# Kernel optimization log

Hardware: AMD Instinct MI355X
Metric: run time of the kernel (lower is better)

The kernel has to match this reference:

```python
import jax, jax.numpy as jnp
import numpy as np
import itertools

N = 600000
CIN = 64
COUT = 64
KS = 3
STRIDE = 2
DIL = 1
GRID = 256        # coordinate range before striding
M = 512           # per-axis key radix (fits int32 keys for batch<=2)
SHIFT = (KS - 1) // 2 * DIL   # keeps shifted coords non-negative under neighbor offsets
SENT = 2 ** 30    # sentinel key for padded unique slots
BN_EPS = 1e-5

OFFSETS = list(itertools.product(range(-(KS // 2), KS // 2 + 1), repeat=3))  # 27 offsets, row-major


def setup_inputs() -> dict:
    key = jax.random.key(0)
    k1, k2, k3, k4, k5, k6, k7, k8 = jax.random.split(key, 8)
    xyz = jax.random.randint(k1, (N, 3), 0, GRID, dtype=jnp.int32)
    b = jax.random.randint(k2, (N, 1), 0, 2, dtype=jnp.int32)  # batch of 2 scenes
    coords = jnp.concatenate([xyz, b], axis=1)                 # [N,4] = (x,y,z,batch)
    feats = jax.random.normal(k3, (N, CIN), dtype=jnp.float32)
    weight = jax.random.normal(k4, (27, CIN, COUT), dtype=jnp.float32) / np.sqrt(27 * CIN)
    bn_scale = jax.random.uniform(k5, (COUT,), jnp.float32, 0.5, 1.5)
    bn_bias = jax.random.normal(k6, (COUT,), jnp.float32) * 0.1
    bn_mean = jax.random.normal(k7, (COUT,), jnp.float32) * 0.1
    bn_var = jax.random.uniform(k8, (COUT,), jnp.float32, 0.5, 1.5)
    return {"coords": coords, "feats": feats, "weight": weight,
            "bn_scale": bn_scale, "bn_bias": bn_bias, "bn_mean": bn_mean, "bn_var": bn_var}


def _encode(xyz, b):
    # pack (batch, x, y, z) into a single sortable int32 key
    return ((b * M + xyz[:, 0] + SHIFT) * M + (xyz[:, 1] + SHIFT)) * M + (xyz[:, 2] + SHIFT)


def _forward(coords, feats, weight, bn_scale, bn_bias, bn_mean, bn_var):
    # --- stride path: voxel downsample via unique + scatter-add (index_add) ---
    xyz = coords[:, :3] // STRIDE
    b = coords[:, 3]
    keys = _encode(xyz, b)                                   # [N]
    ukeys, inv = jnp.unique(keys, size=N, fill_value=SENT, return_inverse=True)  # sorted, padded
    fds = jax.ops.segment_sum(feats, inv, num_segments=N)    # pooled feats [N, CIN]
    valid = ukeys < SENT                                      # real (non-padded) voxels

    # --- sparse 3x3x3 conv at stride 1 (output coords == input coords) ---
    # gather(neighbor) -> matmul(W_k) -> accumulate, per kernel offset
    out = jnp.zeros((N, COUT), dtype=feats.dtype)
    for k, (dx, dy, dz) in enumerate(OFFSETS):
        delta = ((dx * M) + dy) * M + dz
        q = ukeys + delta * DIL
        pos = jnp.clip(jnp.searchsorted(ukeys, q), 0, N - 1)
        match = (ukeys[pos] == q) & valid
        gathered = jnp.where(match[:, None], fds[pos], 0.0)   # [N, CIN]
        out = out + gathered @ weight[k]

    # --- BatchNorm (eval-mode running stats) + ReLU ---
    inv_std = jax.lax.rsqrt(bn_var + BN_EPS)
    out = (out - bn_mean) * (bn_scale * inv_std) + bn_bias
    out = jax.nn.relu(out)
    return jnp.where(valid[:, None], out, 0.0)                # zero padded rows


def reference(coords, feats, weight, bn_scale, bn_bias, bn_mean, bn_var):
    return _forward(coords, feats, weight, bn_scale, bn_bias, bn_mean, bn_var)
```

## Files before the change

kernel.cpp:

```cpp
#include <hip/hip_runtime.h>
#include <hip/hip_bf16.h>

#define NPTS 600000
#define NKEYS (1 << 22)
#define CHUNK 4096
#define NPART (NKEYS / CHUNK)

typedef unsigned int u32;
typedef unsigned short u16;
typedef __attribute__((ext_vector_type(8))) short short8;
typedef __attribute__((ext_vector_type(4))) float f32x4;

__device__ __forceinline__ u16 f2bf(float x) {
  union { float f; u32 u; } c; c.f = x;
  u32 r = c.u + 0x7fffu + ((c.u >> 16) & 1u);
  return (u16)(r >> 16);
}

__global__ void k0a_bn(const float* __restrict__ s, const float* __restrict__ b,
                       const float* __restrict__ m, const float* __restrict__ v,
                       float* __restrict__ ab) {
  int c = threadIdx.x;
  float a = s[c] * rsqrtf(v[c] + 1e-5f);
  ab[c] = a;
  ab[64 + c] = b[c] - m[c] * a;
}

__global__ void k0b_wt(const float* __restrict__ W, u16* __restrict__ Wt) {
  int e = blockIdx.x * 256 + threadIdx.x;
  if (e >= 27 * 4096) return;
  int k = e >> 12, rem = e & 4095, cin = rem >> 6, cout = rem & 63;
  Wt[(k << 12) + (cout << 6) + cin] = f2bf(W[e]);
}

__global__ void k1_keys(const int* __restrict__ coords, int* __restrict__ keys,
                        u32* __restrict__ lut) {
  int i = blockIdx.x * 256 + threadIdx.x;
  if (i >= NPTS) return;
  int4 c4 = *(const int4*)(coords + i * 4);
  int k = (c4.w << 21) | ((c4.x >> 1) << 14) | ((c4.y >> 1) << 7) | (c4.z >> 1);
  keys[i] = k;
  atomicAdd(&lut[k], 1u);
}

__global__ void k2a_part(const u32* __restrict__ lut, u32* __restrict__ partials) {
  __shared__ u32 sd[256];
  int blk = blockIdx.x, t = threadIdx.x;
  const u32* p = lut + blk * CHUNK;
  u32 s = 0;
  for (int j = t; j < CHUNK; j += 256) s += (p[j] != 0u);
  sd[t] = s; __syncthreads();
  for (int o = 128; o > 0; o >>= 1) { if (t < o) sd[t] += sd[t + o]; __syncthreads(); }
  if (t == 0) partials[blk] = sd[0];
}

__global__ void k2b_top(u32* __restrict__ partials) {
  __shared__ u32 sh[NPART];
  int t = threadIdx.x;
  u32 x = partials[t];
  sh[t] = x; __syncthreads();
  for (int off = 1; off < NPART; off <<= 1) {
    u32 add = (t >= off) ? sh[t - off] : 0u;
    __syncthreads();
    sh[t] += add;
    __syncthreads();
  }
  partials[t] = sh[t] - x;
  if (t == NPART - 1) partials[NPART] = sh[t];
}

__global__ void k2c_fill(u32* __restrict__ lut, const u32* __restrict__ partials,
                         int* __restrict__ r2k, float* __restrict__ fds32) {
  __shared__ u32 tsum[256];
  int blk = blockIdx.x, t = threadIdx.x;
  int base = blk * CHUNK + t * 16;
  u32 loc[16]; u32 s = 0;
#pragma unroll
  for (int j = 0; j < 16; j++) { loc[j] = lut[base + j]; s += (loc[j] != 0u); }
  tsum[t] = s; __syncthreads();
  for (int off = 1; off < 256; off <<= 1) {
    u32 add = (t >= off) ? tsum[t - off] : 0u;
    __syncthreads();
    tsum[t] += add;
    __syncthreads();
  }
  u32 rank = partials[blk] + tsum[t] - s;
#pragma unroll
  for (int j = 0; j < 16; j++) {
    if (loc[j]) {
      u32 flag = (loc[j] > 1u) ? 0x80000000u : 0u;
      lut[base + j] = (rank + 1u) | flag;
      r2k[rank] = base + j;
      if (flag) {
        float4 z = {0.f, 0.f, 0.f, 0.f};
        float* d = fds32 + ((size_t)rank << 6);
#pragma unroll
        for (int c = 0; c < 16; c++) *(float4*)(d + c * 4) = z;
      }
      rank++;
    } else lut[base + j] = 0u;
  }
}

__global__ void k3_seg(const float* __restrict__ feats, const int* __restrict__ keys,
                       const u32* __restrict__ lut, float* __restrict__ fds32,
                       u16* __restrict__ fdsb) {
  int idx = blockIdx.x * 256 + threadIdx.x;
  if (idx >= NPTS * 16) return;
  int i = idx >> 4, q = (idx & 15) << 2;
  u32 lv = lut[keys[i]];
  u32 r = (lv & 0x7fffffffu) - 1u;
  float4 v = *(const float4*)(feats + (size_t)i * 64 + q);
  if (lv >> 31) {
    float* dst = fds32 + ((size_t)r << 6) + q;
    atomicAdd(dst + 0, v.x); atomicAdd(dst + 1, v.y);
    atomicAdd(dst + 2, v.z); atomicAdd(dst + 3, v.w);
  } else {
    ushort4 o;
    o.x = f2bf(v.x); o.y = f2bf(v.y); o.z = f2bf(v.z); o.w = f2bf(v.w);
    *(ushort4*)(fdsb + ((size_t)r << 6) + q) = o;
  }
}

__global__ void k3b_fix(const int* __restrict__ r2k, const u32* __restrict__ lut,
                        const u32* __restrict__ pU,
                        const float* __restrict__ fds32, u16* __restrict__ fdsb) {
  int idx = blockIdx.x * 256 + threadIdx.x;
  int r = idx >> 2;
  if (r >= (int)(*pU)) return;
  u32 lv = lut[r2k[r]];
  if (!(lv >> 31)) return;
  int q = (idx & 3) << 4;
  const float* src = fds32 + ((size_t)r << 6) + q;
  u16* dst = fdsb + ((size_t)r << 6) + q;
#pragma unroll
  for (int j = 0; j < 4; j++) {
    float4 v = *(const float4*)(src + j * 4);
    ushort4 o;
    o.x = f2bf(v.x); o.y = f2bf(v.y); o.z = f2bf(v.z); o.w = f2bf(v.w);
    *(ushort4*)(dst + j * 4) = o;
  }
}

__global__ __launch_bounds__(320) void k4_conv(
    const u32* __restrict__ lut, const int* __restrict__ r2k,
    const u16* __restrict__ fdsb, const u16* __restrict__ Wt,
    const u32* __restrict__ pU, const float* __restrict__ ab,
    float* __restrict__ out) {
  __shared__ __align__(16) char ldsA[2][8192];
  const u32 U = *pU;
  int tid = threadIdx.x;
  int w = tid >> 6, l = tid & 63;
  int bid = blockIdx.x;
  int cpx = (int)gridDim.x >> 3;
  int swz = (bid & 7) * cpx + (bid >> 3);
  int rbase = swz * 64;

  int key = -1, x = 0, y = 0, z = 0;
  if (w == 0) {
    int r = rbase + l;
    key = ((u32)r < U) ? r2k[r] : -1;
    z = key & 127; y = (key >> 7) & 127; x = (key >> 14) & 127;
  }
  u32 lvr[4];
  short8 rg[2][8];
  const short8 z8 = {0, 0, 0, 0, 0, 0, 0, 0};

#define PROBE(T) { \
    const int dx_ = (T) / 9 - 1, dy_ = ((T) / 3) % 3 - 1, dz_ = (T) % 3 - 1; \
    int nx_ = x + dx_, ny_ = y + dy_, nz_ = z + dz_; \
    bool ok_ = (key >= 0) & ((u32)nx_ < 128u) & ((u32)ny_ < 128u) & ((u32)nz_ < 128u); \
    int a_ = ok_ ? (key + dx_ * 16384 + dy_ * 128 + dz_) : NKEYS; \
    lvr[(T) & 3] = lut[a_]; }

#define LOADRG(T) { \
    u32 lv_ = lvr[(T) & 3]; \
    _Pragma("unroll") for (int j = 0; j < 8; j++) rg[(T) & 1][j] = z8; \
    if (lv_) { \
      const u16* fr_ = fdsb + ((size_t)((lv_ & 0x7fffffffu) - 1u) << 6); \
      _Pragma("unroll") for (int j = 0; j < 8; j++) \
        rg[(T) & 1][j] = *(const short8*)(fr_ + j * 8); } }

#define DSW(T) { \
    char* dst_ = &ldsA[(T) & 1][l * 128]; \
    int r7_ = l & 7; \
    _Pragma("unroll") for (int j = 0; j < 8; j++) \
      *(short8*)(dst_ + (((j + r7_) & 7) << 4)) = rg[(T) & 1][j]; }

  int ct = w - 1;
  int col = l & 15, kg = l >> 4;
  f32x4 acc[4] = {};

  if (w == 0) {
    PROBE(0) PROBE(1) PROBE(2) PROBE(3)
    LOADRG(0)
    DSW(0)
    LOADRG(1)
  }
  asm volatile("" ::: "memory");
  asm volatile("s_waitcnt lgkmcnt(0)" ::: "memory");
  __builtin_amdgcn_s_barrier();
  asm volatile("" ::: "memory");

#pragma unroll
  for (int k = 0; k < 27; k++) {
    if (w == 0) {
      if (k + 1 < 27) DSW(k + 1)
      if (k + 2 < 27) LOADRG(k + 2)
      if (k + 4 < 27) PROBE(k + 4)
    } else {
      const u16* wk = Wt + (k << 12) + (((ct << 4) + col) << 6) + (kg << 3);
      short8 b0 = *(const short8*)(wk);
      short8 b1 = *(const short8*)(wk + 32);
      const char* slab = &ldsA[k & 1][0];
#pragma unroll
      for (int rt = 0; rt < 4; rt++) {
        int row = (rt << 4) + col;
        const char* rp = slab + row * 128;
        int r7 = row & 7;
        short8 a0 = *(const short8*)(rp + (((kg + r7) & 7) << 4));
        short8 a1 = *(const short8*)(rp + (((kg + 4 + r7) & 7) << 4));
        acc[rt] = __builtin_amdgcn_mfma_f32_16x16x32_bf16(a0, b0, acc[rt], 0, 0, 0);
        acc[rt] = __builtin_amdgcn_mfma_f32_16x16x32_bf16(a1, b1, acc[rt], 0, 0, 0);
      }
    }
    asm volatile("" ::: "memory");
    asm volatile("s_waitcnt lgkmcnt(0)" ::: "memory");
    __builtin_amdgcn_s_barrier();
    asm volatile("" ::: "memory");
  }
#undef PROBE
#undef LOADRG
#undef DSW

  if (w > 0) {
    int c = (ct << 4) | col;
    float al = ab[c], be = ab[64 + c];
#pragma unroll
    for (int rt = 0; rt < 4; rt++) {
#pragma unroll
      for (int i = 0; i < 4; i++) {
        int r = rbase + (rt << 4) + (kg << 2) + i;
        if (r >= NPTS) continue;
        bool valid = ((u32)r < U);
        float vv = 0.f;
        if (valid) {
          vv = fmaf(acc[rt][i], al, be);
          vv = vv > 0.f ? vv : 0.f;
        }
        out[((size_t)r << 6) + c] = vv;
      }
    }
  }
}

extern "C" void kernel_launch(void* const* d_in, const int* in_sizes, int n_in,
                              void* d_out, int out_size, void* d_ws, size_t ws_size,
                              hipStream_t stream) {
  const int*   coords = (const int*)d_in[0];
  const float* feats  = (const float*)d_in[1];
  const float* W      = (const float*)d_in[2];
  const float* bns    = (const float*)d_in[3];
  const float* bnb    = (const float*)d_in[4];
  const float* bnm    = (const float*)d_in[5];
  const float* bnv    = (const float*)d_in[6];
  float* out = (float*)d_out;

  char* ws = (char*)d_ws;
  size_t off = 0;
  auto alloc = [&](size_t bytes) -> void* {
    void* p = ws + off;
    off += (bytes + 255) & ~(size_t)255;
    return p;
  };
  u32* lut      = (u32*)alloc((size_t)(NKEYS + 1) * 4);
  u32* partials = (u32*)alloc((NPART + 8) * 4);
  int* keys     = (int*)alloc((size_t)NPTS * 4);
  int* r2k      = (int*)alloc((size_t)NPTS * 4);
  u16* fdsb     = (u16*)alloc((size_t)(NPTS + 1) * 64 * 2);
  u16* Wt       = (u16*)alloc((size_t)27 * 4096 * 2);
  float* ab     = (float*)alloc(128 * 4);
  (void)ws_size; (void)out_size; (void)n_in; (void)in_sizes;

  float* fds32 = out;

  hipMemsetAsync(lut, 0, (size_t)(NKEYS + 1) * 4, stream);

  k0a_bn<<<1, 64, 0, stream>>>(bns, bnb, bnm, bnv, ab);
  k0b_wt<<<(27 * 4096 + 255) / 256, 256, 0, stream>>>(W, Wt);
  k1_keys<<<(NPTS + 255) / 256, 256, 0, stream>>>(coords, keys, lut);
  k2a_part<<<NPART, 256, 0, stream>>>(lut, partials);
  k2b_top<<<1, NPART, 0, stream>>>(partials);
  k2c_fill<<<NPART, 256, 0, stream>>>(lut, partials, r2k, fds32);
  k3_seg<<<(NPTS * 16 + 255) / 256, 256, 0, stream>>>(feats, keys, lut, fds32, fdsb);
  k3b_fix<<<(NPTS * 4 + 255) / 256, 256, 0, stream>>>(r2k, lut, partials + NPART, fds32, fdsb);
  k4_conv<<<(NPTS + 63) / 64, 320, 0, stream>>>(lut, r2k, fdsb, Wt,
                                                partials + NPART, ab, out);
}
```

Measured before the change: 590.8 us.

## Use direct global-to-LDS loads with a 5-stage ring for conv gathers

The producer wave now issues buffer global_load_lds instructions that write gathered neighbor feature rows straight into LDS, replacing the register round trip and separate LDS store. The double buffer becomes a five-slot ring so loads run three offsets ahead, tracked by explicit vmcnt waits. Rows with no neighbor point at a zeroed pad row, which removes the branch. The LDS layout changes from a swizzled row-major form to a column-chunk-major form that matches the direct-load pattern. LDS use grows to 40KB per block, which may lower occupancy, and the hand-counted waits are fragile.

```diff
diff --git a/kernel.cpp b/kernel.cpp
--- a/kernel.cpp
+++ b/kernel.cpp
@@ -147,7 +147,7 @@
     const u16* __restrict__ fdsb, const u16* __restrict__ Wt,
     const u32* __restrict__ pU, const float* __restrict__ ab,
     float* __restrict__ out) {
-  __shared__ __align__(16) char ldsA[2][8192];
+  __shared__ __align__(16) char ldsA[5][8192];
   const u32 U = *pU;
   int tid = threadIdx.x;
   int w = tid >> 6, l = tid & 63;
@@ -163,8 +163,6 @@
     z = key & 127; y = (key >> 7) & 127; x = (key >> 14) & 127;
   }
   u32 lvr[4];
-  short8 rg[2][8];
-  const short8 z8 = {0, 0, 0, 0, 0, 0, 0, 0};
 
 #define PROBE(T) { \
     const int dx_ = (T) / 9 - 1, dy_ = ((T) / 3) % 3 - 1, dz_ = (T) % 3 - 1; \
@@ -173,65 +171,74 @@
     int a_ = ok_ ? (key + dx_ * 16384 + dy_ * 128 + dz_) : NKEYS; \
     lvr[(T) & 3] = lut[a_]; }
 
-#define LOADRG(T) { \
+#define GLD(T) { \
     u32 lv_ = lvr[(T) & 3]; \
-    _Pragma("unroll") for (int j = 0; j < 8; j++) rg[(T) & 1][j] = z8; \
-    if (lv_) { \
-      const u16* fr_ = fdsb + ((size_t)((lv_ & 0x7fffffffu) - 1u) << 6); \
-      _Pragma("unroll") for (int j = 0; j < 8; j++) \
-        rg[(T) & 1][j] = *(const short8*)(fr_ + j * 8); } }
-
-#define DSW(T) { \
-    char* dst_ = &ldsA[(T) & 1][l * 128]; \
-    int r7_ = l & 7; \
-    _Pragma("unroll") for (int j = 0; j < 8; j++) \
-      *(short8*)(dst_ + (((j + r7_) & 7) << 4)) = rg[(T) & 1][j]; }
+    u32 row_ = lv_ ? ((lv_ & 0x7fffffffu) - 1u) : (u32)NPTS; \
+    const char* fr_ = (const char*)(fdsb + ((size_t)row_ << 6)); \
+    char* sl_ = &ldsA[(T) % 5][0]; \
+    __builtin_amdgcn_global_load_lds((const __attribute__((address_space(1))) void*)(fr_ +   0), (__attribute__((address_space(3))) void*)(sl_ +    0), 16, 0, 0); \
+    __builtin_amdgcn_global_load_lds((const __attribute__((address_space(1))) void*)(fr_ +  16), (__attribute__((address_space(3))) void*)(sl_ + 1024), 16, 0, 0); \
+    __builtin_amdgcn_global_load_lds((const __attribute__((address_space(1))) void*)(fr_ +  32), (__attribute__((address_space(3))) void*)(sl_ + 2048), 16, 0, 0); \
+    __builtin_amdgcn_global_load_lds((const __attribute__((address_space(1))) void*)(fr_ +  48), (__attribute__((address_space(3))) void*)(sl_ + 3072), 16, 0, 0); \
+    __builtin_amdgcn_global_load_lds((const __attribute__((address_space(1))) void*)(fr_ +  64), (__attribute__((address_space(3))) void*)(sl_ + 4096), 16, 0, 0); \
+    __builtin_amdgcn_global_load_lds((const __attribute__((address_space(1))) void*)(fr_ +  80), (__attribute__((address_space(3))) void*)(sl_ + 5120), 16, 0, 0); \
+    __builtin_amdgcn_global_load_lds((const __attribute__((address_space(1))) void*)(fr_ +  96), (__attribute__((address_space(3))) void*)(sl_ + 6144), 16, 0, 0); \
+    __builtin_amdgcn_global_load_lds((const __attribute__((address_space(1))) void*)(fr_ + 112), (__attribute__((address_space(3))) void*)(sl_ + 7168), 16, 0, 0); }
 
   int ct = w - 1;
   int col = l & 15, kg = l >> 4;
   f32x4 acc[4] = {};
 
+#define CONSUME(K) { \
+    const char* sl_ = &ldsA[(K) % 5][0]; \
+    const u16* wk_ = Wt + ((K) << 12) + (((ct << 4) + col) << 6) + (kg << 3); \
+    short8 b0_ = *(const short8*)(wk_); \
+    short8 b1_ = *(const short8*)(wk_ + 32); \
+    short8 a0_[4], a1_[4]; \
+    _Pragma("unroll") for (int rt = 0; rt < 4; rt++) { \
+      int row_ = (rt << 4) + col; \
+      a0_[rt] = *(const short8*)(sl_ + (kg << 10) + (row_ << 4)); \
+      a1_[rt] = *(const short8*)(sl_ + ((kg + 4) << 10) + (row_ << 4)); } \
+    _Pragma("unroll") for (int rt = 0; rt < 4; rt++) { \
+      acc[rt] = __builtin_amdgcn_mfma_f32_16x16x32_bf16(a0_[rt], b0_, acc[rt], 0, 0, 0); \
+      acc[rt] = __builtin_amdgcn_mfma_f32_16x16x32_bf16(a1_[rt], b1_, acc[rt], 0, 0, 0); } }
+
+#define NWAIT(K) ( (((K)-1) < 24 ? 8 : 0) + (((K)-1) < 21 ? 1 : 0) + \
+                   (((K)     < 24) ? 8 : 0) + (((K)     < 21) ? 1 : 0) )
+
+#define BODY(K) { \
+    if (w == 0) { \
+      if ((K) + 3 < 27) GLD((K) + 3) \
+      if ((K) + 6 < 27) PROBE((K) + 6) \
+      asm volatile("s_waitcnt vmcnt(%0)" :: "n"(NWAIT(K)) : "memory"); \
+    } else { \
+      CONSUME(K) \
+    } \
+    asm volatile("" ::: "memory"); \
+    __builtin_amdgcn_s_barrier(); \
+    asm volatile("" ::: "memory"); }
+
   if (w == 0) {
     PROBE(0) PROBE(1) PROBE(2) PROBE(3)
-    LOADRG(0)
-    DSW(0)
-    LOADRG(1)
+    asm volatile("s_waitcnt vmcnt(0)" ::: "memory");
+    GLD(0)
+    asm volatile("s_waitcnt vmcnt(0)" ::: "memory");
+    PROBE(4) GLD(1) PROBE(5) GLD(2)
   }
   asm volatile("" ::: "memory");
-  asm volatile("s_waitcnt lgkmcnt(0)" ::: "memory");
   __builtin_amdgcn_s_barrier();
   asm volatile("" ::: "memory");
 
-#pragma unroll
-  for (int k = 0; k < 27; k++) {
-    if (w == 0) {
-      if (k + 1 < 27) DSW(k + 1)
-      if (k + 2 < 27) LOADRG(k + 2)
-      if (k + 4 < 27) PROBE(k + 4)
-    } else {
-      const u16* wk = Wt + (k << 12) + (((ct << 4) + col) << 6) + (kg << 3);
-      short8 b0 = *(const short8*)(wk);
-      short8 b1 = *(const short8*)(wk + 32);
-      const char* slab = &ldsA[k & 1][0];
-#pragma unroll
-      for (int rt = 0; rt < 4; rt++) {
-        int row = (rt << 4) + col;
-        const char* rp = slab + row * 128;
-        int r7 = row & 7;
-        short8 a0 = *(const short8*)(rp + (((kg + r7) & 7) << 4));
-        short8 a1 = *(const short8*)(rp + (((kg + 4 + r7) & 7) << 4));
-        acc[rt] = __builtin_amdgcn_mfma_f32_16x16x32_bf16(a0, b0, acc[rt], 0, 0, 0);
-        acc[rt] = __builtin_amdgcn_mfma_f32_16x16x32_bf16(a1, b1, acc[rt], 0, 0, 0);
-      }
-    }
-    asm volatile("" ::: "memory");
-    asm volatile("s_waitcnt lgkmcnt(0)" ::: "memory");
-    __builtin_amdgcn_s_barrier();
-    asm volatile("" ::: "memory");
-  }
+  BODY(0)  BODY(1)  BODY(2)  BODY(3)  BODY(4)  BODY(5)  BODY(6)
+  BODY(7)  BODY(8)  BODY(9)  BODY(10) BODY(11) BODY(12) BODY(13)
+  BODY(14) BODY(15) BODY(16) BODY(17) BODY(18) BODY(19) BODY(20)
+  BODY(21) BODY(22) BODY(23) BODY(24) BODY(25) BODY(26)
+
 #undef PROBE
-#undef LOADRG
-#undef DSW
+#undef GLD
+#undef CONSUME
+#undef NWAIT
+#undef BODY
 
   if (w > 0) {
     int c = (ct << 4) | col;
@@ -285,6 +292,7 @@
   float* fds32 = out;
 
   hipMemsetAsync(lut, 0, (size_t)(NKEYS + 1) * 4, stream);
+  hipMemsetAsync(fdsb + (size_t)NPTS * 64, 0, 128, stream);
 
   k0a_bn<<<1, 64, 0, stream>>>(bns, bnb, bnm, bnv, ab);
   k0b_wt<<<(27 * 4096 + 255) / 256, 256, 0, stream>>>(W, Wt);
```

New measurement: 557.1 us. 5.7% less time.
